# Performance work log

Hardware: AMD Instinct MI355X
Metric: run time of the kernel (lower is better)

The kernel has to match this reference:

```python
import jax, jax.numpy as jnp
import numpy as np

N, S, E = 50000, 16, 400000
D, EDIM = 128, 64
H, K = 4, 32          # n_head, per-head output_dim
NMP, DEPTH = 2, 2


def attn_agg(x, neigh, Wq, Wk, Wv):
    # x: [n, D], neigh: [n, s, D], W*: [H, D, K]
    q = jnp.einsum('nd,hdk->nhk', x, Wq)
    k = jnp.einsum('nsd,hdk->nshk', neigh, Wk)
    v = jnp.einsum('nsd,hdk->nshk', neigh, Wv)
    scale = jnp.asarray(1.0 / np.sqrt(K), x.dtype)
    scores = jnp.einsum('nhk,nshk->nhs', q, k) * scale
    attn = jax.nn.softmax(scores, axis=-1)
    out = jax.nn.elu(jnp.einsum('nhs,nshk->nhk', attn, v))  # activation per head
    return out.reshape(out.shape[0], H * K)                  # concat heads


def setup_inputs():
    key = jax.random.key(0)
    ks = jax.random.split(key, 14)
    sD, sE = 1.0 / np.sqrt(D), 1.0 / np.sqrt(EDIM)
    return {
        'feats': jax.random.normal(ks[0], (N, D), jnp.float32),
        'node_emb': jax.random.normal(ks[1], (N, D), jnp.float32) * 0.02,
        'Wprep': jax.random.normal(ks[2], (D, D), jnp.float32) * sD,
        'edge_emb': jax.random.normal(ks[3], (NMP, E, EDIM), jnp.float32),
        'Wedgeprep': jax.random.normal(ks[4], (NMP, EDIM, D), jnp.float32) * sE,
        'Wq_e': jax.random.normal(ks[5], (NMP, DEPTH, H, D, K), jnp.float32) * sD,
        'Wk_e': jax.random.normal(ks[6], (NMP, DEPTH, H, D, K), jnp.float32) * sD,
        'Wv_e': jax.random.normal(ks[7], (NMP, DEPTH, H, D, K), jnp.float32) * sD,
        'Wq_n': jax.random.normal(ks[8], (NMP, DEPTH, H, D, K), jnp.float32) * sD,
        'Wk_n': jax.random.normal(ks[9], (NMP, DEPTH, H, D, K), jnp.float32) * sD,
        'Wv_n': jax.random.normal(ks[10], (NMP, DEPTH, H, D, K), jnp.float32) * sD,
        'node2edge_idx': jax.random.randint(ks[11], (NMP, N, S), 0, E, jnp.int32),
        'edge_node_adj': jax.random.randint(ks[12], (NMP, E, 2), 0, N, jnp.int32),
    }


def reference(feats, node_emb, Wprep, edge_emb, Wedgeprep,
              Wq_e, Wk_e, Wv_e, Wq_n, Wk_n, Wv_n,
              node2edge_idx, edge_node_adj):
    outputs = []
    for mp in range(NMP):
        f = jax.lax.stop_gradient(feats)           # feats[all_ids].detach()
        dummy_feats = node_emb                      # prep layer_idx=0 (id embedding)
        all_feats = f @ Wprep                       # prep layer_idx=1
        all_edges = edge_emb[mp] @ Wedgeprep[mp]    # edge_prep[mp], shuffle=False
        skip = []
        for l in range(DEPTH):
            # --- edge update: gather 2 endpoint node feats per edge ---
            en = all_feats[edge_node_adj[mp]]       # [E, 2, D]
            next_edges = attn_agg(all_edges, en, Wq_e[mp, l], Wk_e[mp, l], Wv_e[mp, l])
            # --- node update: gather S incident edge feats per node (OLD edges) ---
            x = dummy_feats if l == 0 else all_feats
            ne = all_edges[node2edge_idx[mp]]       # [N, S, D]
            next_feats = attn_agg(x, ne, Wq_n[mp, l], Wk_n[mp, l], Wv_n[mp, l])
            skip.append(next_feats)
            all_feats, all_edges = next_feats, next_edges
        outputs.append(jnp.concatenate(skip, axis=-1))  # [N, DEPTH*H*K]
    return jnp.stack(outputs, axis=0)                   # [NMP, N, DEPTH*H*K]
```

## Files before the change

### kernel.cpp

```cpp
#include <hip/hip_runtime.h>

#define N_NODES 50000
#define S_NEI 16
#define E_EDGES 400000
#define DDIM 128
#define EDIMC 64
#define NMPC 2
#define DEPTHC 2

typedef __attribute__((ext_vector_type(8))) short short8v;
typedef __attribute__((ext_vector_type(4))) float float4v;

__device__ __forceinline__ unsigned short f2bf(float f) {
  unsigned int u = __float_as_uint(f);
  unsigned int r = (u + 0x7fffu + ((u >> 16) & 1u)) >> 16;
  return (unsigned short)r;
}
__device__ __forceinline__ float bf2f(unsigned short h) { return __uint_as_float((unsigned int)h << 16); }
__device__ __forceinline__ float bfs(short h) { return bf2f((unsigned short)h); }

__global__ void build_wt(const float* __restrict__ Wprep, const float* __restrict__ Wedgeprep,
                         const float* __restrict__ Wq_e, const float* __restrict__ Wk_e,
                         const float* __restrict__ Wv_e, const float* __restrict__ Wq_n,
                         const float* __restrict__ Wk_n, const float* __restrict__ Wv_n,
                         unsigned short* __restrict__ WT) {
  int idx = blockIdx.x * 256 + threadIdx.x;
  if (idx >= 27 * 16384) return;
  int slot = idx >> 14, r = idx & 16383;
  float v = 0.f;
  if (slot < 24) {
    int ml = slot / 6, mat = slot % 6;
    int c = r >> 7, d = r & 127;
    int h = c >> 5, kk = c & 31;
    const float* W = (mat == 0) ? Wk_e : (mat == 1) ? Wv_e : (mat == 2) ? Wq_n
                   : (mat == 3) ? Wq_e : (mat == 4) ? Wk_n : Wv_n;
    v = W[(((size_t)ml * 4 + h) * 128 + d) * 32 + kk];
  } else if (slot == 24) {
    int c = r >> 7, d = r & 127;
    v = Wprep[d * 128 + c];
  } else {
    int mp = slot - 25;
    int c = r >> 6, k = r & 63;
    if (c < 128) v = Wedgeprep[((size_t)mp * 64 + k) * 128 + c];
  }
  WT[idx] = f2bf(v);
}

__global__ void build_qk(const float* __restrict__ Wq_n, const float* __restrict__ Wk_n,
                         unsigned short* __restrict__ QT) {
  int idx = blockIdx.x * 256 + threadIdx.x;
  int mh = idx >> 14, r = idx & 16383;
  int cp = r >> 7, d = r & 127;
  const float* q = Wq_n + ((size_t)mh * 128 + d) * 32;
  const float* k = Wk_n + ((size_t)mh * 128 + cp) * 32;
  float s = 0.f;
  #pragma unroll
  for (int j = 0; j < 32; ++j) s += q[j] * k[j];
  QT[idx] = f2bf(s);
}

__global__ void build_wv(const float* __restrict__ Wv_n, unsigned short* __restrict__ WV) {
  int idx = blockIdx.x * 256 + threadIdx.x;
  int ml = idx >> 14, r14 = idx & 16383;
  int r = r14 >> 7, d = r14 & 127;
  int h = r >> 5, kp = r & 31;
  WV[idx] = f2bf(Wv_n[(((size_t)ml * 4 + h) * 128 + d) * 32 + kp]);
}

template<int KDIM, int NW, bool ASPLIT>
__global__ __launch_bounds__(256, 3)
void proj(const unsigned short* __restrict__ Xbf, const float* __restrict__ Xf,
          const unsigned short* __restrict__ WT,
          unsigned short* __restrict__ Y0, unsigned short* __restrict__ Y1,
          unsigned short* __restrict__ Y2, unsigned short* __restrict__ Y3,
          int rs0, int rs1, int rs2, int rs3, int M) {
  constexpr int NKK  = KDIM / 32;
  constexpr int CHPR = KDIM / 8;
  constexpr int SWZ  = CHPR - 1;
  __shared__ unsigned short Wl[128 * KDIM];
  const int tid  = threadIdx.x;
  const int lane = tid & 63;
  const int wv   = tid >> 6;
  const int l15  = lane & 15, lg = lane >> 4;
  const long m0  = (long)blockIdx.x * 128 + wv * 32;

  short8v xb[2][NKK];
  #pragma unroll
  for (int rf = 0; rf < 2; ++rf) {
    long row = m0 + rf * 16 + l15; if (row >= M) row = M - 1;
    #pragma unroll
    for (int kk = 0; kk < NKK; ++kk) {
      const int k0 = kk * 32 + lg * 8;
      if (ASPLIT) {
        const float* p = Xf + row * KDIM + k0;
        float4v a0 = *(const float4v*)p;
        float4v a1 = *(const float4v*)(p + 4);
        #pragma unroll
        for (int j = 0; j < 8; ++j) {
          float x = (j < 4) ? a0[j] : a1[j - 4];
          xb[rf][kk][j] = (short)f2bf(x);
        }
      } else {
        xb[rf][kk] = *(const short8v*)(Xbf + row * KDIM + k0);
      }
    }
  }

  unsigned short* Ys[4] = {Y0, Y1, Y2, Y3};
  const int rsv[4] = {rs0, rs1, rs2, rs3};
  #pragma unroll
  for (int w = 0; w < NW; ++w) {
    if (w) __syncthreads();
    {
      const uint4* src = (const uint4*)(WT + (size_t)w * 16384);
      #pragma unroll
      for (int i = 0; i < CHPR / 2; ++i) {
        int ci = i * 256 + tid;
        int row = ci / CHPR, ch = ci & SWZ;
        uint4 v = src[ci];
        *(uint4*)((char*)Wl + row * (KDIM * 2) + ((ch ^ (row & SWZ)) << 4)) = v;
      }
    }
    __syncthreads();

    float4v acc[8][2];
    #pragma unroll
    for (int cf = 0; cf < 8; ++cf)
      #pragma unroll
      for (int rf = 0; rf < 2; ++rf) acc[cf][rf] = (float4v)0.f;

    #pragma unroll
    for (int kk = 0; kk < NKK; ++kk) {
      #pragma unroll
      for (int cf = 0; cf < 8; ++cf) {
        const int row = cf * 16 + l15;
        const int ch  = (kk * 4 + lg) ^ (row & SWZ);
        short8v b = *(const short8v*)((char*)Wl + row * (KDIM * 2) + (ch << 4));
        acc[cf][0] = __builtin_amdgcn_mfma_f32_16x16x32_bf16(b, xb[0][kk], acc[cf][0], 0, 0, 0);
        acc[cf][1] = __builtin_amdgcn_mfma_f32_16x16x32_bf16(b, xb[1][kk], acc[cf][1], 0, 0, 0);
      }
    }

    #pragma unroll
    for (int rf = 0; rf < 2; ++rf) {
      const long m = m0 + rf * 16 + l15;
      if (m < M) {
        #pragma unroll
        for (int cf = 0; cf < 8; ++cf) {
          const int c0 = cf * 16 + lg * 4;
          float4v a = acc[cf][rf];
          ushort4 o;
          o.x = f2bf(a[0]); o.y = f2bf(a[1]); o.z = f2bf(a[2]); o.w = f2bf(a[3]);
          *(ushort4*)(Ys[w] + m * (long)rsv[w] + c0) = o;
        }
      }
    }
  }
}

template<int PREP>
__global__ __launch_bounds__(512, 4)
void edge_fused(unsigned short* __restrict__ eold, const unsigned short* __restrict__ WTq,
                const unsigned short* __restrict__ KVn, const int* __restrict__ adj,
                unsigned short* __restrict__ enew,
                const float* __restrict__ emb, const unsigned short* __restrict__ WTprep) {
  __shared__ unsigned short Wl[128 * 128];
  const int tid  = threadIdx.x;
  const int lane = tid & 63;
  const int wv   = tid >> 6;
  const int l15  = lane & 15, lg = lane >> 4;
  const long m0  = (long)blockIdx.x * 128 + wv * 16;

  const long e = m0 + l15;
  const int2 nn = *(const int2*)(adj + e * 2);
  const size_t b0 = (size_t)nn.x * 256, b1 = (size_t)nn.y * 256;

  short8v xb[4];
  if (PREP) {
    {
      const uint4* src = (const uint4*)WTprep;
      #pragma unroll
      for (int i = 0; i < 2; ++i) {
        int ci = i * 512 + tid;
        int row = ci >> 3, ch = ci & 7;
        uint4 v = src[ci];
        *(uint4*)((char*)Wl + row * 128 + ((ch ^ (row & 7)) << 4)) = v;
      }
    }
    short8v eb[2];
    {
      const long row = m0 + l15;
      #pragma unroll
      for (int kk = 0; kk < 2; ++kk) {
        const float* p = emb + row * 64 + kk * 32 + lg * 8;
        float4v a0 = *(const float4v*)p;
        float4v a1 = *(const float4v*)(p + 4);
        #pragma unroll
        for (int j = 0; j < 8; ++j) {
          float x = (j < 4) ? a0[j] : a1[j - 4];
          eb[kk][j] = (short)f2bf(x);
        }
      }
    }
    __syncthreads();
    float4v accP[8];
    #pragma unroll
    for (int cf = 0; cf < 8; ++cf) accP[cf] = (float4v)0.f;
    #pragma unroll
    for (int kk = 0; kk < 2; ++kk) {
      #pragma unroll
      for (int cf = 0; cf < 8; ++cf) {
        const int row = cf * 16 + l15;
        const int ch  = (kk * 4 + lg) ^ (row & 7);
        short8v b = *(const short8v*)((char*)Wl + row * 128 + (ch << 4));
        accP[cf] = __builtin_amdgcn_mfma_f32_16x16x32_bf16(b, eb[kk], accP[cf], 0, 0, 0);
      }
    }
    __syncthreads();
    {
      const int er = wv * 16 + l15;
      #pragma unroll
      for (int cf = 0; cf < 8; ++cf) {
        float4v a = accP[cf];
        ushort4 o;
        o.x = f2bf(a[0]); o.y = f2bf(a[1]); o.z = f2bf(a[2]); o.w = f2bf(a[3]);
        const int ch16 = cf * 2 + (lg >> 1);
        const int off  = er * 256 + ((ch16 ^ (er & 15)) << 4) + (lg & 1) * 8;
        *(ushort4*)((char*)Wl + off) = o;
      }
    }
    __syncthreads();
    {
      unsigned short* dst = eold + (size_t)blockIdx.x * 16384;
      #pragma unroll
      for (int i = 0; i < 4; ++i) {
        int c = i * 512 + tid;
        int row = c >> 4, ch = c & 15;
        uint4 v = *(const uint4*)((char*)Wl + row * 256 + ((ch ^ (row & 15)) << 4));
        *(uint4*)(dst + (size_t)c * 8) = v;
      }
    }
    {
      const int row = wv * 16 + l15;
      #pragma unroll
      for (int kk = 0; kk < 4; ++kk) {
        const int ch = (kk * 4 + lg) ^ (row & 15);
        xb[kk] = *(const short8v*)((char*)Wl + row * 256 + (ch << 4));
      }
    }
    __syncthreads();
  } else {
    const long row = m0 + l15;
    #pragma unroll
    for (int kk = 0; kk < 4; ++kk)
      xb[kk] = *(const short8v*)(eold + row * 128 + kk * 32 + lg * 8);
  }

  {
    const uint4* src = (const uint4*)WTq;
    #pragma unroll
    for (int i = 0; i < 4; ++i) {
      int ci = i * 512 + tid;
      int row = ci >> 4, ch = ci & 15;
      uint4 v = src[ci];
      *(uint4*)((char*)Wl + row * 256 + ((ch ^ (row & 15)) << 4)) = v;
    }
  }
  __syncthreads();

  ushort4 gk0[8], gk1[8];
  #pragma unroll
  for (int cf = 0; cf < 8; ++cf) {
    const int c0 = cf * 16 + lg * 4;
    gk0[cf] = *(const ushort4*)(KVn + b0 + c0);
    gk1[cf] = *(const ushort4*)(KVn + b1 + c0);
  }

  float4v accQ[8];
  #pragma unroll
  for (int cf = 0; cf < 8; ++cf) accQ[cf] = (float4v)0.f;
  #pragma unroll
  for (int kk = 0; kk < 4; ++kk) {
    #pragma unroll
    for (int cf = 0; cf < 8; ++cf) {
      const int row = cf * 16 + l15;
      const int ch  = (kk * 4 + lg) ^ (row & 15);
      short8v b = *(const short8v*)((char*)Wl + row * 256 + (ch << 4));
      accQ[cf] = __builtin_amdgcn_mfma_f32_16x16x32_bf16(b, xb[kk], accQ[cf], 0, 0, 0);
    }
  }

  const float scale = 0.17677669529663687f;
  {
    float p0[4] = {0.f, 0.f, 0.f, 0.f}, p1[4] = {0.f, 0.f, 0.f, 0.f};
    #pragma unroll
    for (int cf = 0; cf < 8; ++cf) {
      const int h = cf >> 1;
      ushort4 k0 = gk0[cf];
      ushort4 k1 = gk1[cf];
      float4v q = accQ[cf];
      p0[h] += q[0] * bf2f(k0.x) + q[1] * bf2f(k0.y) + q[2] * bf2f(k0.z) + q[3] * bf2f(k0.w);
      p1[h] += q[0] * bf2f(k1.x) + q[1] * bf2f(k1.y) + q[2] * bf2f(k1.z) + q[3] * bf2f(k1.w);
    }
    float a0[4], a1[4];
    #pragma unroll
    for (int h = 0; h < 4; ++h) {
      p0[h] += __shfl_xor(p0[h], 16); p0[h] += __shfl_xor(p0[h], 32);
      p1[h] += __shfl_xor(p1[h], 16); p1[h] += __shfl_xor(p1[h], 32);
      const float s0 = p0[h] * scale, s1 = p1[h] * scale;
      const float mx = fmaxf(s0, s1);
      const float e0 = __expf(s0 - mx), e1 = __expf(s1 - mx);
      const float inv = 1.0f / (e0 + e1);
      a0[h] = e0 * inv; a1[h] = e1 * inv;
    }
    #pragma unroll
    for (int cf = 0; cf < 8; ++cf) {
      const int c0 = cf * 16 + lg * 4;
      const int h = cf >> 1;
      ushort4 v0 = *(const ushort4*)(KVn + b0 + 128 + c0);
      ushort4 v1 = *(const ushort4*)(KVn + b1 + 128 + c0);
      float o[4];
      o[0] = a0[h] * bf2f(v0.x) + a1[h] * bf2f(v1.x);
      o[1] = a0[h] * bf2f(v0.y) + a1[h] * bf2f(v1.y);
      o[2] = a0[h] * bf2f(v0.z) + a1[h] * bf2f(v1.z);
      o[3] = a0[h] * bf2f(v0.w) + a1[h] * bf2f(v1.w);
      o[0] = o[0] > 0.f ? o[0] : expm1f(o[0]);
      o[1] = o[1] > 0.f ? o[1] : expm1f(o[1]);
      o[2] = o[2] > 0.f ? o[2] : expm1f(o[2]);
      o[3] = o[3] > 0.f ? o[3] : expm1f(o[3]);
      ushort4 ob;
      ob.x = f2bf(o[0]); ob.y = f2bf(o[1]); ob.z = f2bf(o[2]); ob.w = f2bf(o[3]);
      *(ushort4*)(enew + e * 128 + c0) = ob;
    }
  }
}

__global__ __launch_bounds__(256, 2)
void node_attn(const unsigned short* __restrict__ qt, const unsigned short* __restrict__ eold,
               const int* __restrict__ n2e, unsigned short* __restrict__ Z) {
  const int lane = threadIdx.x & 63;
  const long n = (long)blockIdx.x * 4 + (threadIdx.x >> 6);
  const short8v qv = *(const short8v*)(qt + n * 512 + lane * 8);
  const int i8 = (lane & 15) * 8;
  short8v xk[16];
  #pragma unroll
  for (int s = 0; s < 16; ++s) {
    const long e = n2e[n * 16 + s];
    xk[s] = *(const short8v*)(eold + e * 128 + i8);
  }
  float sc[16];
  #pragma unroll
  for (int s = 0; s < 16; ++s) {
    float p = 0.f;
    #pragma unroll
    for (int j = 0; j < 8; ++j) p += bfs(qv[j]) * bfs(xk[s][j]);
    p += __shfl_xor(p, 1); p += __shfl_xor(p, 2);
    p += __shfl_xor(p, 4); p += __shfl_xor(p, 8);
    sc[s] = p * 0.17677669529663687f;
  }
  float m = sc[0];
  #pragma unroll
  for (int s = 1; s < 16; ++s) m = fmaxf(m, sc[s]);
  float sum = 0.f;
  #pragma unroll
  for (int s = 0; s < 16; ++s) { sc[s] = __expf(sc[s] - m); sum += sc[s]; }
  const float inv = 1.0f / sum;
  float z[8] = {0.f, 0.f, 0.f, 0.f, 0.f, 0.f, 0.f, 0.f};
  #pragma unroll
  for (int s = 0; s < 16; ++s)
    #pragma unroll
    for (int j = 0; j < 8; ++j) z[j] += sc[s] * bfs(xk[s][j]);
  ushort4 o0, o1;
  o0.x = f2bf(z[0] * inv); o0.y = f2bf(z[1] * inv); o0.z = f2bf(z[2] * inv); o0.w = f2bf(z[3] * inv);
  o1.x = f2bf(z[4] * inv); o1.y = f2bf(z[5] * inv); o1.z = f2bf(z[6] * inv); o1.w = f2bf(z[7] * inv);
  *(ushort4*)(Z + n * 512 + lane * 8) = o0;
  *(ushort4*)(Z + n * 512 + lane * 8 + 4) = o1;
}

__global__ __launch_bounds__(256, 2)
void node_post(const unsigned short* __restrict__ Zb, const unsigned short* __restrict__ WV,
               unsigned short* __restrict__ fnext, float* __restrict__ outp, int M) {
  __shared__ unsigned short Wl[128 * 128];
  const int tid  = threadIdx.x;
  const int lane = tid & 63;
  const int wv   = tid >> 6;
  const int l15  = lane & 15, lg = lane >> 4;
  const long m0  = (long)blockIdx.x * 128 + wv * 32;
  {
    const uint4* src = (const uint4*)WV;
    #pragma unroll
    for (int i = 0; i < 8; ++i) {
      int ci = i * 256 + tid;
      int row = ci >> 4, ch = ci & 15;
      uint4 v = src[ci];
      *(uint4*)((char*)Wl + row * 256 + ((ch ^ (row & 15)) << 4)) = v;
    }
  }
  __syncthreads();

  #pragma unroll
  for (int h = 0; h < 4; ++h) {
    float4v acc[2][2];
    #pragma unroll
    for (int cf = 0; cf < 2; ++cf)
      #pragma unroll
      for (int rf = 0; rf < 2; ++rf) acc[cf][rf] = (float4v)0.f;
    #pragma unroll
    for (int rf = 0; rf < 2; ++rf) {
      long row = m0 + rf * 16 + l15; if (row >= M) row = M - 1;
      #pragma unroll
      for (int kk = 0; kk < 4; ++kk) {
        short8v zb = *(const short8v*)(Zb + row * 512 + h * 128 + kk * 32 + lg * 8);
        #pragma unroll
        for (int cf = 0; cf < 2; ++cf) {
          const int arow = h * 32 + cf * 16 + l15;
          const int ch = (kk * 4 + lg) ^ (arow & 15);
          short8v b = *(const short8v*)((char*)Wl + arow * 256 + (ch << 4));
          acc[cf][rf] = __builtin_amdgcn_mfma_f32_16x16x32_bf16(b, zb, acc[cf][rf], 0, 0, 0);
        }
      }
    }
    #pragma unroll
    for (int rf = 0; rf < 2; ++rf) {
      const long m = m0 + rf * 16 + l15;
      if (m < M) {
        #pragma unroll
        for (int cf = 0; cf < 2; ++cf) {
          const int c0 = h * 32 + cf * 16 + lg * 4;
          float o[4];
          #pragma unroll
          for (int j = 0; j < 4; ++j) {
            float a = acc[cf][rf][j];
            o[j] = a > 0.f ? a : expm1f(a);
          }
          ushort4 ob;
          ob.x = f2bf(o[0]); ob.y = f2bf(o[1]); ob.z = f2bf(o[2]); ob.w = f2bf(o[3]);
          *(ushort4*)(fnext + m * 128 + c0) = ob;
          float4 of; of.x = o[0]; of.y = o[1]; of.z = o[2]; of.w = o[3];
          *(float4*)(outp + m * 256 + c0) = of;
        }
      }
    }
  }
}

extern "C" void kernel_launch(void* const* d_in, const int* in_sizes, int n_in,
                              void* d_out, int out_size, void* d_ws, size_t ws_size,
                              hipStream_t stream) {
  const float* feats     = (const float*)d_in[0];
  const float* node_emb  = (const float*)d_in[1];
  const float* Wprep     = (const float*)d_in[2];
  const float* edge_emb  = (const float*)d_in[3];
  const float* Wedgeprep = (const float*)d_in[4];
  const float* Wq_e      = (const float*)d_in[5];
  const float* Wk_e      = (const float*)d_in[6];
  const float* Wv_e      = (const float*)d_in[7];
  const float* Wq_n      = (const float*)d_in[8];
  const float* Wk_n      = (const float*)d_in[9];
  const float* Wv_n      = (const float*)d_in[10];
  const int*   n2e       = (const int*)d_in[11];
  const int*   adj       = (const int*)d_in[12];
  float* out = (float*)d_out;

  char* w = (char*)d_ws;
  auto carve = [&](size_t bytes) -> char* {
    char* p = w; w += (bytes + 255) & ~(size_t)255; return p;
  };
  unsigned short* e_a   = (unsigned short*)carve((size_t)E_EDGES * 128 * 2);
  unsigned short* e_b   = (unsigned short*)carve((size_t)E_EDGES * 128 * 2);
  unsigned short* fprep = (unsigned short*)carve((size_t)N_NODES * 128 * 2);
  unsigned short* fa    = (unsigned short*)carve((size_t)N_NODES * 128 * 2);
  unsigned short* fb    = (unsigned short*)carve((size_t)N_NODES * 128 * 2);
  unsigned short* KVn   = (unsigned short*)carve((size_t)N_NODES * 256 * 2);
  unsigned short* qt    = (unsigned short*)carve((size_t)N_NODES * 512 * 2);
  unsigned short* Zb    = (unsigned short*)carve((size_t)N_NODES * 512 * 2);
  unsigned short* WT    = (unsigned short*)carve((size_t)27 * 16384 * 2);
  unsigned short* QT    = (unsigned short*)carve((size_t)16 * 16384 * 2);
  unsigned short* WV    = (unsigned short*)carve((size_t)4 * 16384 * 2);

  build_wt<<<(27 * 16384 + 255) / 256, 256, 0, stream>>>(
      Wprep, Wedgeprep, Wq_e, Wk_e, Wv_e, Wq_n, Wk_n, Wv_n, WT);
  build_qk<<<16 * 64, 256, 0, stream>>>(Wq_n, Wk_n, QT);
  build_wv<<<4 * 64, 256, 0, stream>>>(Wv_n, WV);

  const int gN = (N_NODES + 127) / 128;
  const int gE = E_EDGES / 128;

  proj<128, 1, true><<<gN, 256, 0, stream>>>(
      nullptr, feats, WT + (size_t)24 * 16384, fprep, nullptr, nullptr, nullptr,
      128, 0, 0, 0, N_NODES);

  for (int mp = 0; mp < NMPC; ++mp) {
    unsigned short *ecur = e_a, *enext = e_b;
    unsigned short *fchi = fprep, *fnhi = fa;
    for (int l = 0; l < DEPTHC; ++l) {
      const int ml = mp * 2 + l;
      const unsigned short* base = WT + (size_t)ml * 6 * 16384;
      const unsigned short* qkb  = QT + (size_t)ml * 4 * 16384;
      proj<128, 2, false><<<gN, 256, 0, stream>>>(
          fchi, nullptr, base, KVn, KVn + 128, nullptr, nullptr,
          256, 256, 0, 0, N_NODES);
      if (l == 0) {
        proj<128, 4, true><<<gN, 256, 0, stream>>>(
            nullptr, node_emb, qkb, qt, qt + 128, qt + 256, qt + 384,
            512, 512, 512, 512, N_NODES);
      } else {
        proj<128, 4, false><<<gN, 256, 0, stream>>>(
            fchi, nullptr, qkb, qt, qt + 128, qt + 256, qt + 384,
            512, 512, 512, 512, N_NODES);
      }
      if (l == 0) {
        edge_fused<1><<<gE, 512, 0, stream>>>(
            ecur, base + (size_t)3 * 16384, KVn, adj + (size_t)mp * E_EDGES * 2, enext,
            edge_emb + (size_t)mp * E_EDGES * EDIMC, WT + (size_t)(25 + mp) * 16384);
      } else {
        edge_fused<0><<<gE, 512, 0, stream>>>(
            ecur, base + (size_t)3 * 16384, KVn, adj + (size_t)mp * E_EDGES * 2, enext,
            nullptr, nullptr);
      }
      node_attn<<<N_NODES / 4, 256, 0, stream>>>(
          qt, ecur, n2e + (size_t)mp * N_NODES * S_NEI, Zb);
      node_post<<<gN, 256, 0, stream>>>(
          Zb, WV + (size_t)ml * 16384, fnhi,
          out + (size_t)mp * N_NODES * 256 + (size_t)l * 128, N_NODES);

      unsigned short* t = ecur; ecur = enext; enext = t;
      fchi = fnhi; fnhi = fb;
    }
  }
}
```

Baseline: 1.238 ms.

## Fuse node attention with value projection and prefetch edge V loads

Merges node_attn and node_post into a single node_fused kernel. The per-head attention-weighted edge sum is kept in shared memory as fp32 and multiplied by a transposed, swizzled Wv tile with scalar FMAs. This drops the bf16 Zb intermediate buffer, its global round trip and one launch per layer. In exchange, each 4-node block reloads the full Wv matrix into LDS and the projection runs on CUDA-core FMAs instead of MFMA. Separately, edge_fused now issues its V gathers together with the K gathers, raising register pressure in exchange for earlier memory issue.

```diff
diff --git a/kernel.cpp b/kernel.cpp
--- a/kernel.cpp
+++ b/kernel.cpp
@@ -7,6 +7,9 @@
 #define EDIMC 64
 #define NMPC 2
 #define DEPTHC 2
+
+#define HSS 4360
+#define KSS 136
 
 typedef __attribute__((ext_vector_type(8))) short short8v;
 typedef __attribute__((ext_vector_type(4))) float float4v;
@@ -61,9 +64,8 @@
 
 __global__ void build_wv(const float* __restrict__ Wv_n, unsigned short* __restrict__ WV) {
   int idx = blockIdx.x * 256 + threadIdx.x;
-  int ml = idx >> 14, r14 = idx & 16383;
-  int r = r14 >> 7, d = r14 & 127;
-  int h = r >> 5, kp = r & 31;
+  int ml = idx >> 14, r = idx & 16383;
+  int h = r >> 12, kp = (r >> 7) & 31, d = r & 127;
   WV[idx] = f2bf(Wv_n[(((size_t)ml * 4 + h) * 128 + d) * 32 + kp]);
 }
 
@@ -268,12 +270,14 @@
   }
   __syncthreads();
 
-  ushort4 gk0[8], gk1[8];
+  ushort4 gk0[8], gk1[8], gv0[8], gv1[8];
   #pragma unroll
   for (int cf = 0; cf < 8; ++cf) {
     const int c0 = cf * 16 + lg * 4;
     gk0[cf] = *(const ushort4*)(KVn + b0 + c0);
     gk1[cf] = *(const ushort4*)(KVn + b1 + c0);
+    gv0[cf] = *(const ushort4*)(KVn + b0 + 128 + c0);
+    gv1[cf] = *(const ushort4*)(KVn + b1 + 128 + c0);
   }
 
   float4v accQ[8];
@@ -317,8 +321,8 @@
     for (int cf = 0; cf < 8; ++cf) {
       const int c0 = cf * 16 + lg * 4;
       const int h = cf >> 1;
-      ushort4 v0 = *(const ushort4*)(KVn + b0 + 128 + c0);
-      ushort4 v1 = *(const ushort4*)(KVn + b1 + 128 + c0);
+      ushort4 v0 = gv0[cf];
+      ushort4 v1 = gv1[cf];
       float o[4];
       o[0] = a0[h] * bf2f(v0.x) + a1[h] * bf2f(v1.x);
       o[1] = a0[h] * bf2f(v0.y) + a1[h] * bf2f(v1.y);
@@ -336,17 +340,35 @@
 }
 
 __global__ __launch_bounds__(256, 2)
-void node_attn(const unsigned short* __restrict__ qt, const unsigned short* __restrict__ eold,
-               const int* __restrict__ n2e, unsigned short* __restrict__ Z) {
-  const int lane = threadIdx.x & 63;
-  const long n = (long)blockIdx.x * 4 + (threadIdx.x >> 6);
+void node_fused(const unsigned short* __restrict__ qt, const unsigned short* __restrict__ eold,
+                const int* __restrict__ n2e, const unsigned short* __restrict__ WVT,
+                unsigned short* __restrict__ fnext, float* __restrict__ outp) {
+  __shared__ unsigned short WvL[4 * HSS];
+  __shared__ float zbuf[4][4][KSS];
+  const int tid  = threadIdx.x;
+  const int lane = tid & 63;
+  const int wv   = tid >> 6;
+  const long n   = (long)blockIdx.x * 4 + wv;
+  const int g = lane >> 4, i = lane & 15;
+
+  {
+    const uint4* src = (const uint4*)WVT;
+    #pragma unroll
+    for (int t = 0; t < 8; ++t) {
+      int c = t * 256 + tid;
+      int row = c >> 4, cc = c & 15;
+      int h = row >> 5, kp = row & 31;
+      int pos = cc ^ ((row >> 1) & 7);
+      *(uint4*)((char*)WvL + ((size_t)h * HSS + kp * KSS + pos * 8) * 2) = src[c];
+    }
+  }
+
   const short8v qv = *(const short8v*)(qt + n * 512 + lane * 8);
-  const int i8 = (lane & 15) * 8;
   short8v xk[16];
   #pragma unroll
   for (int s = 0; s < 16; ++s) {
     const long e = n2e[n * 16 + s];
-    xk[s] = *(const short8v*)(eold + e * 128 + i8);
+    xk[s] = *(const short8v*)(eold + e * 128 + i * 8);
   }
   float sc[16];
   #pragma unroll
@@ -370,78 +392,33 @@
   for (int s = 0; s < 16; ++s)
     #pragma unroll
     for (int j = 0; j < 8; ++j) z[j] += sc[s] * bfs(xk[s][j]);
-  ushort4 o0, o1;
-  o0.x = f2bf(z[0] * inv); o0.y = f2bf(z[1] * inv); o0.z = f2bf(z[2] * inv); o0.w = f2bf(z[3] * inv);
-  o1.x = f2bf(z[4] * inv); o1.y = f2bf(z[5] * inv); o1.z = f2bf(z[6] * inv); o1.w = f2bf(z[7] * inv);
-  *(ushort4*)(Z + n * 512 + lane * 8) = o0;
-  *(ushort4*)(Z + n * 512 + lane * 8 + 4) = o1;
-}
-
-__global__ __launch_bounds__(256, 2)
-void node_post(const unsigned short* __restrict__ Zb, const unsigned short* __restrict__ WV,
-               unsigned short* __restrict__ fnext, float* __restrict__ outp, int M) {
-  __shared__ unsigned short Wl[128 * 128];
-  const int tid  = threadIdx.x;
-  const int lane = tid & 63;
-  const int wv   = tid >> 6;
-  const int l15  = lane & 15, lg = lane >> 4;
-  const long m0  = (long)blockIdx.x * 128 + wv * 32;
-  {
-    const uint4* src = (const uint4*)WV;
-    #pragma unroll
-    for (int i = 0; i < 8; ++i) {
-      int ci = i * 256 + tid;
-      int row = ci >> 4, ch = ci & 15;
-      uint4 v = src[ci];
-      *(uint4*)((char*)Wl + row * 256 + ((ch ^ (row & 15)) << 4)) = v;
-    }
-  }
+  #pragma unroll
+  for (int j = 0; j < 8; ++j) zbuf[wv][g][i * 8 + j] = z[j] * inv;
   __syncthreads();
 
-  #pragma unroll
-  for (int h = 0; h < 4; ++h) {
-    float4v acc[2][2];
-    #pragma unroll
-    for (int cf = 0; cf < 2; ++cf)
-      #pragma unroll
-      for (int rf = 0; rf < 2; ++rf) acc[cf][rf] = (float4v)0.f;
-    #pragma unroll
-    for (int rf = 0; rf < 2; ++rf) {
-      long row = m0 + rf * 16 + l15; if (row >= M) row = M - 1;
-      #pragma unroll
-      for (int kk = 0; kk < 4; ++kk) {
-        short8v zb = *(const short8v*)(Zb + row * 512 + h * 128 + kk * 32 + lg * 8);
-        #pragma unroll
-        for (int cf = 0; cf < 2; ++cf) {
-          const int arow = h * 32 + cf * 16 + l15;
-          const int ch = (kk * 4 + lg) ^ (arow & 15);
-          short8v b = *(const short8v*)((char*)Wl + arow * 256 + (ch << 4));
-          acc[cf][rf] = __builtin_amdgcn_mfma_f32_16x16x32_bf16(b, zb, acc[cf][rf], 0, 0, 0);
-        }
-      }
-    }
-    #pragma unroll
-    for (int rf = 0; rf < 2; ++rf) {
-      const long m = m0 + rf * 16 + l15;
-      if (m < M) {
-        #pragma unroll
-        for (int cf = 0; cf < 2; ++cf) {
-          const int c0 = h * 32 + cf * 16 + lg * 4;
-          float o[4];
-          #pragma unroll
-          for (int j = 0; j < 4; ++j) {
-            float a = acc[cf][rf][j];
-            o[j] = a > 0.f ? a : expm1f(a);
-          }
-          ushort4 ob;
-          ob.x = f2bf(o[0]); ob.y = f2bf(o[1]); ob.z = f2bf(o[2]); ob.w = f2bf(o[3]);
-          *(ushort4*)(fnext + m * 128 + c0) = ob;
-          float4 of; of.x = o[0]; of.y = o[1]; of.z = o[2]; of.w = o[3];
-          *(float4*)(outp + m * 256 + c0) = of;
-        }
-      }
-    }
-  }
+  const int key = i & 7;
+  const unsigned short* w0p = WvL + (size_t)g * HSS + (2 * i) * KSS;
+  const unsigned short* w1p = w0p + KSS;
+  const float* zz = &zbuf[wv][g][0];
+  float o0 = 0.f, o1 = 0.f;
+  #pragma unroll
+  for (int c = 0; c < 16; ++c) {
+    const int cc = (c ^ key) * 8;
+    float4v z0 = *(const float4v*)(zz + c * 8);
+    float4v z1 = *(const float4v*)(zz + c * 8 + 4);
+    short8v w0 = *(const short8v*)(w0p + cc);
+    short8v w1 = *(const short8v*)(w1p + cc);
+    #pragma unroll
+    for (int j = 0; j < 4; ++j) {
+      o0 += z0[j] * bfs(w0[j]);     o1 += z0[j] * bfs(w1[j]);
+      o0 += z1[j] * bfs(w0[j + 4]); o1 += z1[j] * bfs(w1[j + 4]);
+    }
+  }
+  o0 = o0 > 0.f ? o0 : expm1f(o0);
+  o1 = o1 > 0.f ? o1 : expm1f(o1);
+  ((unsigned int*)fnext)[n * 64 + g * 16 + i] =
+      (unsigned int)f2bf(o0) | ((unsigned int)f2bf(o1) << 16);
+  *(float2*)(outp + n * 256 + g * 32 + 2 * i) = make_float2(o0, o1);
 }
 
 extern "C" void kernel_launch(void* const* d_in, const int* in_sizes, int n_in,
@@ -473,7 +450,6 @@
   unsigned short* fb    = (unsigned short*)carve((size_t)N_NODES * 128 * 2);
   unsigned short* KVn   = (unsigned short*)carve((size_t)N_NODES * 256 * 2);
   unsigned short* qt    = (unsigned short*)carve((size_t)N_NODES * 512 * 2);
-  unsigned short* Zb    = (unsigned short*)carve((size_t)N_NODES * 512 * 2);
   unsigned short* WT    = (unsigned short*)carve((size_t)27 * 16384 * 2);
   unsigned short* QT    = (unsigned short*)carve((size_t)16 * 16384 * 2);
   unsigned short* WV    = (unsigned short*)carve((size_t)4 * 16384 * 2);
@@ -518,11 +494,9 @@
             ecur, base + (size_t)3 * 16384, KVn, adj + (size_t)mp * E_EDGES * 2, enext,
             nullptr, nullptr);
       }
-      node_attn<<<N_NODES / 4, 256, 0, stream>>>(
-          qt, ecur, n2e + (size_t)mp * N_NODES * S_NEI, Zb);
-      node_post<<<gN, 256, 0, stream>>>(
-          Zb, WV + (size_t)ml * 16384, fnhi,
-          out + (size_t)mp * N_NODES * 256 + (size_t)l * 128, N_NODES);
+      node_fused<<<N_NODES / 4, 256, 0, stream>>>(
+          qt, ecur, n2e + (size_t)mp * N_NODES * S_NEI, WV + (size_t)ml * 16384,
+          fnhi, out + (size_t)mp * N_NODES * 256 + (size_t)l * 128);
 
       unsigned short* t = ecur; ecur = enext; enext = t;
       fchi = fnhi; fnhi = fb;
```

New measurement: 1.316 ms. 1.06x slower.
